# Kernel optimization log

Measured on AMD Instinct MI355X. Metric: run time of the kernel, lower is better.

## Reference

```python
import jax, jax.numpy as jnp
import numpy as np

IN_DIM = 1024
HID = 256
OUT_DIM = 1000
NUM_BINS = 51
BATCH = 2048
N_LEGAL = 200


def setup_inputs() -> dict:
    key = jax.random.key(0)
    ks = jax.random.split(key, 12)
    s = lambda fan_in: 1.0 / np.sqrt(fan_in)
    u = lambda k, shp, b: jax.random.uniform(k, shp, jnp.float32, -b, b)
    return {
        "x": jax.random.normal(ks[0], (BATCH, IN_DIM), jnp.float32),
        # weights stored as [in, out] (math-equivalent to torch Linear)
        "w_in": u(ks[1], (IN_DIM, HID), s(IN_DIM)),
        "b_in": u(ks[2], (HID,), s(IN_DIM)),
        "w_ah": u(ks[3], (HID, HID), s(HID)),
        "b_ah": u(ks[4], (HID,), s(HID)),
        "w_ao": u(ks[5], (HID, OUT_DIM * NUM_BINS), s(HID)),
        "b_ao": u(ks[6], (OUT_DIM * NUM_BINS,), s(HID)),
        "w_vh": u(ks[7], (HID, HID), s(HID)),
        "b_vh": u(ks[8], (HID,), s(HID)),
        "w_vo": u(ks[9], (HID, NUM_BINS), s(HID)),
        "b_vo": u(ks[10], (NUM_BINS,), s(HID)),
        "v_range": jnp.linspace(-10.0, 10.0, NUM_BINS, dtype=jnp.float32),
        "possible_moves": jax.random.randint(ks[11], (BATCH, N_LEGAL), 0, OUT_DIM),
    }


def reference(x, w_in, b_in, w_ah, b_ah, w_ao, b_ao, w_vh, b_vh, w_vo, b_vo,
              v_range, possible_moves):
    B = x.shape[0]
    h = jax.nn.relu(x @ w_in + b_in)                       # [B, 256]
    adv_h = jax.nn.relu(h @ w_ah + b_ah)                   # [B, 256]
    val_h = jax.nn.relu(h @ w_vh + b_vh)                   # [B, 256]
    adv = (adv_h @ w_ao + b_ao).reshape(B, OUT_DIM, NUM_BINS)
    val = (val_h @ w_vo + b_vo).reshape(B, 1, NUM_BINS)
    q = val + adv - adv.mean(axis=1, keepdims=True)        # [B, A, bins]
    p = jnp.maximum(jax.nn.softmax(q, axis=2), 1e-5)       # softmax + clamp(min=1e-5)
    q_vals = jnp.sum(p * v_range, axis=2)                  # [B, A]
    # LegalSoftmax: per-row scatter of 1.0 at legal indices, vectorized
    mask = jnp.zeros((B, OUT_DIM), x.dtype).at[
        jnp.arange(B)[:, None], possible_moves].set(1.0)
    filtered = q_vals * mask
    # faithful to torch: any exact-zero entry (masked OR coincidental) -> -inf
    return jnp.where(filtered == 0, -jnp.inf, filtered)
```

## Files before the change

### kernel.cpp

```cpp
#include <hip/hip_runtime.h>
#include <cstdint>
#include <cstddef>

#define NB      2048
#define INDIM   1024
#define HID     256
#define NA      1000
#define BINS    51
#define NLEG    200
#define NPAIR   (NB*NLEG)
#define NBLK    256
#define PPB     (NPAIR/NBLK)

#define NEG_SENTINEL (-1.0e30f)

typedef float    f32x4  __attribute__((ext_vector_type(4)));
typedef __bf16   bf16x8 __attribute__((ext_vector_type(8)));
typedef unsigned short us8 __attribute__((ext_vector_type(8)));
typedef unsigned short us4 __attribute__((ext_vector_type(4)));
typedef unsigned long long u64x2 __attribute__((ext_vector_type(2)));

__device__ __forceinline__ unsigned short f2bf(float f) {
  union { float f; unsigned u; } v; v.f = f;
  return (unsigned short)((v.u + 0x7FFFu + ((v.u >> 16) & 1u)) >> 16);
}
__device__ __forceinline__ bf16x8 as_bf(us8 v) { return __builtin_bit_cast(bf16x8, v); }
__device__ __forceinline__ int imin(int a, int b) { return a < b ? a : b; }

__device__ __forceinline__ unsigned f2fp8x4(float a, float b, float c, float d) {
  int v = 0;
  v = __builtin_amdgcn_cvt_pk_fp8_f32(a, b, v, false);
  v = __builtin_amdgcn_cvt_pk_fp8_f32(c, d, v, true);
  return (unsigned)v;
}
__device__ __forceinline__ unsigned char f2fp8(float f) {
  int v = __builtin_amdgcn_cvt_pk_fp8_f32(f, 0.f, 0, false);
  return (unsigned char)(v & 0xff);
}
__device__ __forceinline__ float fp82f(unsigned char u) {
  return __builtin_amdgcn_cvt_f32_fp8((int)u, 0);
}

__global__ __launch_bounds__(256) void k_pre(
    const float* __restrict__ w_ao, unsigned char* __restrict__ wp8,
    float* __restrict__ wmean_acc,
    const float* __restrict__ w_in, const float* __restrict__ w_ah,
    const float* __restrict__ w_vh,
    unsigned short* __restrict__ w_inT, unsigned short* __restrict__ w_ahT,
    unsigned short* __restrict__ w_vhT,
    float* __restrict__ out, const int* __restrict__ pm,
    int* __restrict__ cnt,
    const float* __restrict__ x, unsigned short* __restrict__ x_bf) {
  __shared__ __align__(16) unsigned char smem[16320];
  int b = blockIdx.x, tid = threadIdx.x;
  if (b < 1000) {
    unsigned char* st = smem;
    int s = b & 7, a0 = (b >> 3) * 8;
    const float* wbase = w_ao + (size_t)(s * 32) * (NA * BINS) + a0 * BINS;
    for (int i = tid; i < 816; i += 256) {
      int kq = i / 102, c4 = i - kq * 102;
      const float* rp = wbase + (size_t)(kq * 4) * (NA * BINS) + c4 * 4;
      float4 f0 = *(const float4*)(rp);
      float4 f1 = *(const float4*)(rp + NA * BINS);
      float4 f2 = *(const float4*)(rp + 2 * NA * BINS);
      float4 f3 = *(const float4*)(rp + 3 * NA * BINS);
      unsigned pk0 = f2fp8x4(f0.x * 16.f, f0.y * 16.f, f0.z * 16.f, f0.w * 16.f);
      unsigned pk1 = f2fp8x4(f1.x * 16.f, f1.y * 16.f, f1.z * 16.f, f1.w * 16.f);
      unsigned pk2 = f2fp8x4(f2.x * 16.f, f2.y * 16.f, f2.z * 16.f, f2.w * 16.f);
      unsigned pk3 = f2fp8x4(f3.x * 16.f, f3.y * 16.f, f3.z * 16.f, f3.w * 16.f);
      unsigned s01lo = __builtin_amdgcn_perm(pk1, pk0, 0x05010400u);
      unsigned s01hi = __builtin_amdgcn_perm(pk1, pk0, 0x07030602u);
      unsigned s23lo = __builtin_amdgcn_perm(pk3, pk2, 0x05010400u);
      unsigned s23hi = __builtin_amdgcn_perm(pk3, pk2, 0x07030602u);
      unsigned o0 = __builtin_amdgcn_perm(s23lo, s01lo, 0x05040100u);
      unsigned o1 = __builtin_amdgcn_perm(s23lo, s01lo, 0x07060302u);
      unsigned o2 = __builtin_amdgcn_perm(s23hi, s01hi, 0x05040100u);
      unsigned o3 = __builtin_amdgcn_perm(s23hi, s01hi, 0x07060302u);
      int k4 = kq * 4;
      int swz = ((c4 >> 2) & 3) << 3;
      int kb = ((k4 & 24) ^ swz) + (k4 & 7);
      int cbase = c4 * 160;
      *(unsigned*)(st + cbase + kb)       = o0;
      *(unsigned*)(st + cbase + 40 + kb)  = o1;
      *(unsigned*)(st + cbase + 80 + kb)  = o2;
      *(unsigned*)(st + cbase + 120 + kb) = o3;
    }
    __syncthreads();
    for (int i = tid; i < 32 * 51; i += 256) {
      int r = i / 51, j = i - r * 51;
      float s8 = 0.f;
#pragma unroll
      for (int aL = 0; aL < 8; aL++) {
        int c = aL * 51 + j;
        s8 += fp82f(st[c * 40 + ((r & 24) ^ (((c >> 4) & 3) << 3)) + (r & 7)]);
      }
      atomicAdd(&wmean_acc[(size_t)(s * 32 + r) * BINS + j], s8);
    }
    int t4 = (tid >> 6) & 3, l = tid & 63;
    int col = t4 * 16 + (l & 15), kg = l >> 4;
    for (int aL = 0; aL < 8; aL++) {
      unsigned lo = 0, hi = 0;
      if (col < BINS) {
        int ci = aL * 51 + col;
        unsigned long long v8 = *(const unsigned long long*)(
            st + ci * 40 + ((kg * 8) ^ (((ci >> 4) & 3) << 3)));
        lo = (unsigned)v8; hi = (unsigned)(v8 >> 32);
      }
      uint2 v; v.x = lo; v.y = hi;
      *(uint2*)(wp8 + (size_t)(a0 + aL) * 16384 +
                (size_t)((s * 2 + (t4 >> 1)) * 64 + l) * 16 + (t4 & 1) * 8) = v;
    }
  } else if (b < 1384) {
    int bb = b - 1000;
    float (*tile)[33] = (float(*)[33])smem;
    const float* w; unsigned short* wT; int K, N, kt, nt;
    if (bb < 256)      { w = w_in; wT = w_inT; K = INDIM; N = HID; kt = bb & 31;        nt = bb >> 5; }
    else if (bb < 320) { w = w_ah; wT = w_ahT; K = HID;   N = HID; kt = (bb - 256) & 7; nt = (bb - 256) >> 3; }
    else               { w = w_vh; wT = w_vhT; K = HID;   N = HID; kt = (bb - 320) & 7; nt = (bb - 320) >> 3; }
    int k0 = kt * 32, n0 = nt * 32;
    int cr = tid >> 5, cc = tid & 31;
#pragma unroll
    for (int it = 0; it < 4; it++)
      tile[cr + it * 8][cc] = w[(size_t)(k0 + cr + it * 8) * N + n0 + cc];
    __syncthreads();
#pragma unroll
    for (int it = 0; it < 4; it++)
      wT[(size_t)(n0 + cr + it * 8) * K + k0 + cc] = f2bf(tile[cc][cr + it * 8]);
  } else if (b < 1884) {
    int base = (b - 1384) * 1024 + tid;
    float4 v = {NEG_SENTINEL, NEG_SENTINEL, NEG_SENTINEL, NEG_SENTINEL};
#pragma unroll
    for (int it = 0; it < 4; it++) ((float4*)out)[base + it * 256] = v;
  } else if (b < 2396) {
    int base4 = (b - 1884) * 1024 + tid;
#pragma unroll
    for (int it = 0; it < 4; it++) {
      float4 v = ((const float4*)x)[base4 + it * 256];
      us4 o;
      o[0] = f2bf(v.x); o[1] = f2bf(v.y); o[2] = f2bf(v.z); o[3] = f2bf(v.w);
      ((us4*)x_bf)[base4 + it * 256] = o;
    }
  } else {
    int* lh = (int*)smem;
    int blk = b - 2396;
    for (int i = tid; i < NA; i += 256) lh[i] = 0;
    __syncthreads();
    int base = blk * PPB;
    for (int i = tid; i < PPB; i += 256) atomicAdd(&lh[pm[base + i]], 1);
    __syncthreads();
    for (int a = tid; a < NA; a += 256) {
      int v = lh[a];
      if (v) atomicAdd(&cnt[a], v);
    }
  }
}

__global__ __launch_bounds__(256) void k_mid(
    const unsigned short* __restrict__ x_bf, const unsigned short* __restrict__ w_inT,
    const float* __restrict__ b_in, unsigned short* __restrict__ h_bf,
    const float* __restrict__ w_vo, const float* __restrict__ wmean_acc,
    const float* __restrict__ b_vo, const float* __restrict__ b_ao,
    unsigned short* __restrict__ Wc, float* __restrict__ bias_c,
    const int* __restrict__ cnt, int* __restrict__ off, int* __restrict__ cursor) {
  __shared__ __align__(16) char smem[1024];
  int b = blockIdx.x, tid = threadIdx.x;
  if (b < 512) {
    int w = tid >> 6, l = tid & 63, la = l & 15, g = l >> 4;
    int idx = b * 4 + w;
    int m0 = (idx & 127) * 16, n0 = (idx >> 7) * 16;
    f32x4 acc = {0.f, 0.f, 0.f, 0.f};
    const us8* Bp = (const us8*)(w_inT + (size_t)(n0 + la) * INDIM) + g;
    const us8* Ap = (const us8*)(x_bf + (size_t)(m0 + la) * INDIM) + g;
#pragma unroll 8
    for (int s = 0; s < 32; s++)
      acc = __builtin_amdgcn_mfma_f32_16x16x32_bf16(as_bf(Ap[s * 4]), as_bf(Bp[s * 4]),
                                                    acc, 0, 0, 0);
    float bb = b_in[n0 + la];
#pragma unroll
    for (int r = 0; r < 4; r++) {
      float v = fmaxf(acc[r] + bb, 0.f);
      h_bf[(size_t)(m0 + g * 4 + r) * HID + n0 + la] = f2bf(v);
    }
  } else if (b < 576) {
    float* sred = (float*)smem;
    int n = b - 512, t = tid;
    for (int k = t; k < 512; k += 256) {
      float v = 0.f;
      if (n < BINS)
        v = (k < 256) ? w_vo[(size_t)k * BINS + n]
                      : (-(0.001f / 16.f) * wmean_acc[(size_t)(k - 256) * BINS + n]);
      Wc[(size_t)n * 512 + k] = f2bf(v);
    }
    float acc = 0.f;
    if (n < BINS)
      for (int a = t; a < NA; a += 256) acc += b_ao[(size_t)a * BINS + n];
    sred[t] = acc;
    __syncthreads();
    for (int d = 128; d > 0; d >>= 1) { if (t < d) sred[t] += sred[t + d]; __syncthreads(); }
    if (t == 0) bias_c[n] = (n < BINS) ? (b_vo[n] - 0.001f * sred[0]) : 0.f;
  } else {
    int* s = (int*)smem;
    int t = tid, i0 = 4 * t;
    int v0 = (i0     < NA) ? cnt[i0]     : 0;
    int v1 = (i0 + 1 < NA) ? cnt[i0 + 1] : 0;
    int v2 = (i0 + 2 < NA) ? cnt[i0 + 2] : 0;
    int v3 = (i0 + 3 < NA) ? cnt[i0 + 3] : 0;
    int sum = v0 + v1 + v2 + v3;
    s[t] = sum;
    __syncthreads();
    for (int d = 1; d < 256; d <<= 1) {
      int u = (t >= d) ? s[t - d] : 0;
      __syncthreads();
      s[t] += u;
      __syncthreads();
    }
    int excl = s[t] - sum;
    if (i0     < NA) { off[i0]     = excl;                cursor[i0]     = excl; }
    if (i0 + 1 < NA) { off[i0 + 1] = excl + v0;           cursor[i0 + 1] = excl + v0; }
    if (i0 + 2 < NA) { off[i0 + 2] = excl + v0 + v1;      cursor[i0 + 2] = excl + v0 + v1; }
    if (i0 + 3 < NA) { off[i0 + 3] = excl + v0 + v1 + v2; cursor[i0 + 3] = excl + v0 + v1 + v2; }
  }
}

__global__ __launch_bounds__(256) void k_heads(
    const unsigned short* __restrict__ h,
    const unsigned short* __restrict__ wA, const float* __restrict__ bA,
    const unsigned short* __restrict__ wV, const float* __restrict__ bV,
    const unsigned short* __restrict__ Wc, const float* __restrict__ bias_c,
    unsigned char* __restrict__ Aext8, float* __restrict__ cbuf_f,
    const int* __restrict__ pm, int* __restrict__ cursor, int* __restrict__ rows) {
  __shared__ __align__(16) char smem[16896];
  int b = blockIdx.x, tid = threadIdx.x;
  if (b < 128) {
    unsigned short* aL = (unsigned short*)smem;
    unsigned short* vL = (unsigned short*)smem + 16 * 264;
    int w = tid >> 6, l = tid & 63, la = l & 15, g = l >> 4;
    int m0 = b * 16;
    const us8* Ap = (const us8*)(h + (size_t)(m0 + la) * HID) + g;
    us8 aF[8];
#pragma unroll
    for (int s = 0; s < 8; s++) aF[s] = Ap[s * 4];
#pragma unroll
    for (int part = 0; part < 2; part++) {
      const unsigned short* BT = part ? wV : wA;
      const float* bias = part ? bV : bA;
      unsigned short* oL = part ? vL : aL;
#pragma unroll
      for (int nt = 0; nt < 4; nt++) {
        int n0 = w * 64 + nt * 16;
        f32x4 acc = {0.f, 0.f, 0.f, 0.f};
        const us8* Bp = (const us8*)(BT + (size_t)(n0 + la) * HID) + g;
#pragma unroll
        for (int s = 0; s < 8; s++)
          acc = __builtin_amdgcn_mfma_f32_16x16x32_bf16(as_bf(aF[s]), as_bf(Bp[s * 4]),
                                                        acc, 0, 0, 0);
        float bb = bias[n0 + la];
#pragma unroll
        for (int r = 0; r < 4; r++) {
          float v = fmaxf(acc[r] + bb, 0.f);
          oL[(g * 4 + r) * 264 + n0 + la] = f2bf(v);
          if (part == 0)
            Aext8[(size_t)(m0 + g * 4 + r) * HID + n0 + la] = f2fp8(v);
        }
      }
    }
    __syncthreads();
    int n0c = w * 16;
    f32x4 acc = {0.f, 0.f, 0.f, 0.f};
    const us8* Vp  = (const us8*)(vL + la * 264) + g;
    const us8* Ap2 = (const us8*)(aL + la * 264) + g;
    const us8* BpV = (const us8*)(Wc + (size_t)(n0c + la) * 512) + g;
    const us8* BpA = (const us8*)(Wc + (size_t)(n0c + la) * 512 + 256) + g;
#pragma unroll
    for (int s = 0; s < 8; s++)
      acc = __builtin_amdgcn_mfma_f32_16x16x32_bf16(as_bf(Vp[s * 4]), as_bf(BpV[s * 4]),
                                                    acc, 0, 0, 0);
#pragma unroll
    for (int s = 0; s < 8; s++)
      acc = __builtin_amdgcn_mfma_f32_16x16x32_bf16(as_bf(Ap2[s * 4]), as_bf(BpA[s * 4]),
                                                    acc, 0, 0, 0);
    float bb = bias_c[n0c + la];
#pragma unroll
    for (int r = 0; r < 4; r++)
      cbuf_f[(size_t)(m0 + g * 4 + r) * 64 + n0c + la] = acc[r] + bb;
  } else {
    int* lc = (int*)smem;
    int* lbase = (int*)(smem + 4096);
    int blk = b - 128, t = tid;
    for (int i = t; i < NA; i += 256) lc[i] = 0;
    __syncthreads();
    int pbase = blk * PPB;
    for (int i = t; i < PPB; i += 256) atomicAdd(&lc[pm[pbase + i]], 1);
    __syncthreads();
    for (int i = t; i < NA; i += 256) {
      int v = lc[i];
      lbase[i] = v ? atomicAdd(&cursor[i], v) : 0;
      lc[i] = 0;
    }
    __syncthreads();
    for (int i = t; i < PPB; i += 256) {
      int a = pm[pbase + i];
      int r = atomicAdd(&lc[a], 1);
      rows[lbase[a] + r] = (pbase + i) / NLEG;
    }
  }
}

#define TILE_BODY(TILE, RA_) do {                                              \
  int rA = (RA_);                                                              \
  const long long* Ap = (const long long*)(Aext8 + (size_t)rA * HID) + g;      \
  const float4* cf = (const float4*)(cbuf_f + (size_t)rA * 64);                \
  long long a8[8];                                                             \
  _Pragma("unroll") for (int s = 0; s < 8; s++) a8[s] = Ap[s * 4];             \
  float4 cq0 = cf[g], cq1 = cf[4 + g], cq2 = cf[8 + g], cq3 = cf[12 + g];      \
  f32x4 acc0 = {0.f,0.f,0.f,0.f}, acc1 = {0.f,0.f,0.f,0.f};                    \
  f32x4 acc2 = {0.f,0.f,0.f,0.f}, acc3 = {0.f,0.f,0.f,0.f};                    \
  __builtin_amdgcn_s_setprio(1);                                               \
  _Pragma("unroll") for (int s = 0; s < 8; s++) {                              \
    u64x2 b01 = sBv[(s * 2) * 64 + l];                                         \
    u64x2 b23 = sBv[(s * 2 + 1) * 64 + l];                                     \
    acc0 = __builtin_amdgcn_mfma_f32_16x16x32_fp8_fp8(                         \
        (long long)b01[0], a8[s], acc0, 0, 0, 0);                              \
    acc1 = __builtin_amdgcn_mfma_f32_16x16x32_fp8_fp8(                         \
        (long long)b01[1], a8[s], acc1, 0, 0, 0);                              \
    acc2 = __builtin_amdgcn_mfma_f32_16x16x32_fp8_fp8(                         \
        (long long)b23[0], a8[s], acc2, 0, 0, 0);                              \
    acc3 = __builtin_amdgcn_mfma_f32_16x16x32_fp8_fp8(                         \
        (long long)b23[1], a8[s], acc3, 0, 0, 0);                              \
  }                                                                            \
  __builtin_amdgcn_s_setprio(0);                                               \
  float S = 0.f;                                                               \
  f32x4 e0, e1, e2, e3;                                                        \
  _Pragma("unroll") for (int r = 0; r < 4; r++) {                              \
    e0[r] = __expf(fmaf(acc0[r], 0.0625f, cq0[r] + bao0[r])); S += e0[r];      \
    e1[r] = __expf(fmaf(acc1[r], 0.0625f, cq1[r] + bao1[r])); S += e1[r];      \
    e2[r] = __expf(fmaf(acc2[r], 0.0625f, cq2[r] + bao2[r])); S += e2[r];      \
    e3[r] = __expf(fmaf(acc3[r], 0.0625f, cq3[r] + bao3[r])); S += e3[r];      \
  }                                                                            \
  S += __shfl_xor(S, 16); S += __shfl_xor(S, 32);                              \
  float inv = 1.f / S, qv = 0.f;                                               \
  _Pragma("unroll") for (int r = 0; r < 4; r++) {                              \
    int bin = g * 4 + r;                                                       \
    qv = fmaf(fmaxf(e0[r] * inv, 1e-5f), (float)bin * 0.4f - 10.f, qv);        \
    qv = fmaf(fmaxf(e1[r] * inv, 1e-5f), (float)(bin + 16) * 0.4f - 10.f, qv); \
    qv = fmaf(fmaxf(e2[r] * inv, 1e-5f), (float)(bin + 32) * 0.4f - 10.f, qv); \
    if (bin + 48 < BINS)                                                       \
      qv = fmaf(fmaxf(e3[r] * inv, 1e-5f), (float)(bin + 48) * 0.4f - 10.f, qv); \
  }                                                                            \
  qv += __shfl_xor(qv, 16); qv += __shfl_xor(qv, 32);                          \
  int gi = (TILE) * 16 + la;                                                   \
  if (g == 0 && gi < count)                                                    \
    out[(size_t)rA * NA + a] = (qv == 0.f) ? NEG_SENTINEL : qv;                \
} while (0)

__global__ __launch_bounds__(256) void k_main_mfma(
    const unsigned char* __restrict__ Aext8,
    const float* __restrict__ cbuf_f,
    const unsigned char* __restrict__ wp8,
    const float* __restrict__ b_ao,
    const int* __restrict__ cnt, const int* __restrict__ off,
    const int* __restrict__ rows,
    float* __restrict__ out) {
  __shared__ __align__(16) long long sB8[2048];
  const u64x2* sBv = (const u64x2*)sB8;
  int bx = blockIdx.x;
  int a = (bx & 7) * 125 + (bx >> 3);
  int count = cnt[a];
  int ntiles = (count + 15) >> 4;
  if ((int)(blockIdx.y * 4) >= ntiles) return;
  int tid = threadIdx.x;
  int w = tid >> 6, l = tid & 63, la = l & 15, g = l >> 4;
  int base = off[a];
  int t0 = blockIdx.y * 4 + w;

  int rQ0 = rows[base + imin( t0       * 16 + la, count - 1)];
  int rQ1 = rows[base + imin((t0 + 16) * 16 + la, count - 1)];

  const float* baop = b_ao + (size_t)a * BINS;
  f32x4 bao0, bao1, bao2, bao3;
#pragma unroll
  for (int r = 0; r < 4; r++) {
    int bin = g * 4 + r;
    bao0[r] = baop[bin];
    bao1[r] = baop[bin + 16];
    bao2[r] = baop[bin + 32];
    bao3[r] = (bin + 48 < BINS) ? baop[bin + 48] : NEG_SENTINEL;
  }

  const u64x2* wpa = (const u64x2*)(wp8 + (size_t)a * 16384);
#pragma unroll
  for (int i = 0; i < 4; i++) ((u64x2*)sB8)[tid + i * 256] = wpa[tid + i * 256];
  __syncthreads();

  if (t0      < ntiles) TILE_BODY(t0,      rQ0);
  if (t0 + 16 < ntiles) TILE_BODY(t0 + 16, rQ1);
  for (int tile = t0 + 32; tile < ntiles; tile += 16) {
    int rAt = rows[base + imin(tile * 16 + la, count - 1)];
    TILE_BODY(tile, rAt);
  }
}

extern "C" void kernel_launch(void* const* d_in, const int* in_sizes, int n_in,
                              void* d_out, int out_size, void* d_ws, size_t ws_size,
                              hipStream_t stream) {
  (void)in_sizes; (void)n_in; (void)out_size; (void)ws_size;
  const float* x     = (const float*)d_in[0];
  const float* w_in  = (const float*)d_in[1];
  const float* b_in  = (const float*)d_in[2];
  const float* w_ah  = (const float*)d_in[3];
  const float* b_ah  = (const float*)d_in[4];
  const float* w_ao  = (const float*)d_in[5];
  const float* b_ao  = (const float*)d_in[6];
  const float* w_vh  = (const float*)d_in[7];
  const float* b_vh  = (const float*)d_in[8];
  const float* w_vo  = (const float*)d_in[9];
  const float* b_vo  = (const float*)d_in[10];
  const int*   pm    = (const int*)d_in[12];
  float* out = (float*)d_out;

  char* p = (char*)d_ws;
  unsigned char*  wp8     = (unsigned char*)p;  p += (size_t)NA * 32 * 512;
  unsigned char*  Aext8   = (unsigned char*)p;  p += (size_t)NB * HID;
  unsigned short* h_bf    = (unsigned short*)p; p += (size_t)NB * HID * 2;
  unsigned short* w_inT   = (unsigned short*)p; p += (size_t)HID * INDIM * 2;
  unsigned short* w_ahT   = (unsigned short*)p; p += (size_t)HID * HID * 2;
  unsigned short* w_vhT   = (unsigned short*)p; p += (size_t)HID * HID * 2;
  unsigned short* Wc      = (unsigned short*)p; p += (size_t)64 * 512 * 2;
  unsigned short* x_bf    = (unsigned short*)p; p += (size_t)NB * INDIM * 2;
  float* bias_c = (float*)p; p += 64 * 4;
  float* cbuf_f = (float*)p; p += (size_t)NB * 64 * 4;
  float* wmean  = (float*)p; p += 13056 * 4;
  int* cnt    = (int*)p; p += NA * 4;
  int* off    = (int*)p; p += NA * 4;
  int* cursor = (int*)p; p += (size_t)NA * 4 + 240;
  int* rows   = (int*)p; p += (size_t)NPAIR * 4 + 256;

  hipMemsetAsync(wmean, 0, (13056 + NA) * sizeof(float), stream);

  k_pre<<<2652, 256, 0, stream>>>(w_ao, wp8, wmean, w_in, w_ah, w_vh,
                                  w_inT, w_ahT, w_vhT, out, pm, cnt, x, x_bf);
  k_mid<<<577, 256, 0, stream>>>(x_bf, w_inT, b_in, h_bf,
                                 w_vo, wmean, b_vo, b_ao, Wc, bias_c,
                                 cnt, off, cursor);
  k_heads<<<384, 256, 0, stream>>>(h_bf, w_ahT, b_ah, w_vhT, b_vh,
                                   Wc, bias_c, Aext8, cbuf_f,
                                   pm, cursor, rows);
  k_main_mfma<<<dim3(1000, 4), 256, 0, stream>>>(Aext8, cbuf_f, wp8, b_ao,
                                                 cnt, off, rows, out);
}
```

Baseline: 209.6 us.

## Fuse four pipeline kernels into one persistent cooperative kernel with grid syncs

```diff
diff --git a/kernel.cpp b/kernel.cpp
--- a/kernel.cpp
+++ b/kernel.cpp
@@ -1,6 +1,9 @@
 #include <hip/hip_runtime.h>
+#include <hip/hip_cooperative_groups.h>
 #include <cstdint>
 #include <cstddef>
+
+namespace cg = cooperative_groups;
 
 #define NB      2048
 #define INDIM   1024
@@ -9,8 +12,7 @@
 #define BINS    51
 #define NLEG    200
 #define NPAIR   (NB*NLEG)
-#define NBLK    256
-#define PPB     (NPAIR/NBLK)
+#define PPB     (NPAIR/256)
 
 #define NEG_SENTINEL (-1.0e30f)
 
@@ -41,268 +43,275 @@
   return __builtin_amdgcn_cvt_f32_fp8((int)u, 0);
 }
 
-__global__ __launch_bounds__(256) void k_pre(
+
+__device__ __forceinline__ void body_pack(
+    int b, unsigned char* st, int tid,
     const float* __restrict__ w_ao, unsigned char* __restrict__ wp8,
-    float* __restrict__ wmean_acc,
+    float* __restrict__ wmean_acc) {
+  int s = b & 7, a0 = (b >> 3) * 8;
+  const float* wbase = w_ao + (size_t)(s * 32) * (NA * BINS) + a0 * BINS;
+  for (int i = tid; i < 816; i += 256) {
+    int kq = i / 102, c4 = i - kq * 102;
+    const float* rp = wbase + (size_t)(kq * 4) * (NA * BINS) + c4 * 4;
+    float4 f0 = *(const float4*)(rp);
+    float4 f1 = *(const float4*)(rp + NA * BINS);
+    float4 f2 = *(const float4*)(rp + 2 * NA * BINS);
+    float4 f3 = *(const float4*)(rp + 3 * NA * BINS);
+    unsigned pk0 = f2fp8x4(f0.x * 16.f, f0.y * 16.f, f0.z * 16.f, f0.w * 16.f);
+    unsigned pk1 = f2fp8x4(f1.x * 16.f, f1.y * 16.f, f1.z * 16.f, f1.w * 16.f);
+    unsigned pk2 = f2fp8x4(f2.x * 16.f, f2.y * 16.f, f2.z * 16.f, f2.w * 16.f);
+    unsigned pk3 = f2fp8x4(f3.x * 16.f, f3.y * 16.f, f3.z * 16.f, f3.w * 16.f);
+    unsigned s01lo = __builtin_amdgcn_perm(pk1, pk0, 0x05010400u);
+    unsigned s01hi = __builtin_amdgcn_perm(pk1, pk0, 0x07030602u);
+    unsigned s23lo = __builtin_amdgcn_perm(pk3, pk2, 0x05010400u);
+    unsigned s23hi = __builtin_amdgcn_perm(pk3, pk2, 0x07030602u);
+    unsigned o0 = __builtin_amdgcn_perm(s23lo, s01lo, 0x05040100u);
+    unsigned o1 = __builtin_amdgcn_perm(s23lo, s01lo, 0x07060302u);
+    unsigned o2 = __builtin_amdgcn_perm(s23hi, s01hi, 0x05040100u);
+    unsigned o3 = __builtin_amdgcn_perm(s23hi, s01hi, 0x07060302u);
+    int k4 = kq * 4;
+    int swz = ((c4 >> 2) & 3) << 3;
+    int kb = ((k4 & 24) ^ swz) + (k4 & 7);
+    int cbase = c4 * 160;
+    *(unsigned*)(st + cbase + kb)       = o0;
+    *(unsigned*)(st + cbase + 40 + kb)  = o1;
+    *(unsigned*)(st + cbase + 80 + kb)  = o2;
+    *(unsigned*)(st + cbase + 120 + kb) = o3;
+  }
+  __syncthreads();
+  for (int i = tid; i < 32 * 51; i += 256) {
+    int r = i / 51, j = i - r * 51;
+    float s8 = 0.f;
+#pragma unroll
+    for (int aL = 0; aL < 8; aL++) {
+      int c = aL * 51 + j;
+      s8 += fp82f(st[c * 40 + ((r & 24) ^ (((c >> 4) & 3) << 3)) + (r & 7)]);
+    }
+    atomicAdd(&wmean_acc[(size_t)(s * 32 + r) * BINS + j], s8);
+  }
+  int t4 = (tid >> 6) & 3, l = tid & 63;
+  int col = t4 * 16 + (l & 15), kg = l >> 4;
+  for (int aL = 0; aL < 8; aL++) {
+    unsigned lo = 0, hi = 0;
+    if (col < BINS) {
+      int ci = aL * 51 + col;
+      unsigned long long v8 = *(const unsigned long long*)(
+          st + ci * 40 + ((kg * 8) ^ (((ci >> 4) & 3) << 3)));
+      lo = (unsigned)v8; hi = (unsigned)(v8 >> 32);
+    }
+    uint2 v; v.x = lo; v.y = hi;
+    *(uint2*)(wp8 + (size_t)(a0 + aL) * 16384 +
+              (size_t)((s * 2 + (t4 >> 1)) * 64 + l) * 16 + (t4 & 1) * 8) = v;
+  }
+}
+
+__device__ __forceinline__ void body_transpose(
+    int bb, unsigned char* smem, int tid,
     const float* __restrict__ w_in, const float* __restrict__ w_ah,
     const float* __restrict__ w_vh,
     unsigned short* __restrict__ w_inT, unsigned short* __restrict__ w_ahT,
-    unsigned short* __restrict__ w_vhT,
-    float* __restrict__ out, const int* __restrict__ pm,
-    int* __restrict__ cnt,
-    const float* __restrict__ x, unsigned short* __restrict__ x_bf) {
-  __shared__ __align__(16) unsigned char smem[16320];
-  int b = blockIdx.x, tid = threadIdx.x;
-  if (b < 1000) {
-    unsigned char* st = smem;
-    int s = b & 7, a0 = (b >> 3) * 8;
-    const float* wbase = w_ao + (size_t)(s * 32) * (NA * BINS) + a0 * BINS;
-    for (int i = tid; i < 816; i += 256) {
-      int kq = i / 102, c4 = i - kq * 102;
-      const float* rp = wbase + (size_t)(kq * 4) * (NA * BINS) + c4 * 4;
-      float4 f0 = *(const float4*)(rp);
-      float4 f1 = *(const float4*)(rp + NA * BINS);
-      float4 f2 = *(const float4*)(rp + 2 * NA * BINS);
-      float4 f3 = *(const float4*)(rp + 3 * NA * BINS);
-      unsigned pk0 = f2fp8x4(f0.x * 16.f, f0.y * 16.f, f0.z * 16.f, f0.w * 16.f);
-      unsigned pk1 = f2fp8x4(f1.x * 16.f, f1.y * 16.f, f1.z * 16.f, f1.w * 16.f);
-      unsigned pk2 = f2fp8x4(f2.x * 16.f, f2.y * 16.f, f2.z * 16.f, f2.w * 16.f);
-      unsigned pk3 = f2fp8x4(f3.x * 16.f, f3.y * 16.f, f3.z * 16.f, f3.w * 16.f);
-      unsigned s01lo = __builtin_amdgcn_perm(pk1, pk0, 0x05010400u);
-      unsigned s01hi = __builtin_amdgcn_perm(pk1, pk0, 0x07030602u);
-      unsigned s23lo = __builtin_amdgcn_perm(pk3, pk2, 0x05010400u);
-      unsigned s23hi = __builtin_amdgcn_perm(pk3, pk2, 0x07030602u);
-      unsigned o0 = __builtin_amdgcn_perm(s23lo, s01lo, 0x05040100u);
-      unsigned o1 = __builtin_amdgcn_perm(s23lo, s01lo, 0x07060302u);
-      unsigned o2 = __builtin_amdgcn_perm(s23hi, s01hi, 0x05040100u);
-      unsigned o3 = __builtin_amdgcn_perm(s23hi, s01hi, 0x07060302u);
-      int k4 = kq * 4;
-      int swz = ((c4 >> 2) & 3) << 3;
-      int kb = ((k4 & 24) ^ swz) + (k4 & 7);
-      int cbase = c4 * 160;
-      *(unsigned*)(st + cbase + kb)       = o0;
-      *(unsigned*)(st + cbase + 40 + kb)  = o1;
-      *(unsigned*)(st + cbase + 80 + kb)  = o2;
-      *(unsigned*)(st + cbase + 120 + kb) = o3;
-    }
-    __syncthreads();
-    for (int i = tid; i < 32 * 51; i += 256) {
-      int r = i / 51, j = i - r * 51;
-      float s8 = 0.f;
-#pragma unroll
-      for (int aL = 0; aL < 8; aL++) {
-        int c = aL * 51 + j;
-        s8 += fp82f(st[c * 40 + ((r & 24) ^ (((c >> 4) & 3) << 3)) + (r & 7)]);
-      }
-      atomicAdd(&wmean_acc[(size_t)(s * 32 + r) * BINS + j], s8);
-    }
-    int t4 = (tid >> 6) & 3, l = tid & 63;
-    int col = t4 * 16 + (l & 15), kg = l >> 4;
-    for (int aL = 0; aL < 8; aL++) {
-      unsigned lo = 0, hi = 0;
-      if (col < BINS) {
-        int ci = aL * 51 + col;
-        unsigned long long v8 = *(const unsigned long long*)(
-            st + ci * 40 + ((kg * 8) ^ (((ci >> 4) & 3) << 3)));
-        lo = (unsigned)v8; hi = (unsigned)(v8 >> 32);
-      }
-      uint2 v; v.x = lo; v.y = hi;
-      *(uint2*)(wp8 + (size_t)(a0 + aL) * 16384 +
-                (size_t)((s * 2 + (t4 >> 1)) * 64 + l) * 16 + (t4 & 1) * 8) = v;
-    }
-  } else if (b < 1384) {
-    int bb = b - 1000;
-    float (*tile)[33] = (float(*)[33])smem;
-    const float* w; unsigned short* wT; int K, N, kt, nt;
-    if (bb < 256)      { w = w_in; wT = w_inT; K = INDIM; N = HID; kt = bb & 31;        nt = bb >> 5; }
-    else if (bb < 320) { w = w_ah; wT = w_ahT; K = HID;   N = HID; kt = (bb - 256) & 7; nt = (bb - 256) >> 3; }
-    else               { w = w_vh; wT = w_vhT; K = HID;   N = HID; kt = (bb - 320) & 7; nt = (bb - 320) >> 3; }
-    int k0 = kt * 32, n0 = nt * 32;
-    int cr = tid >> 5, cc = tid & 31;
-#pragma unroll
-    for (int it = 0; it < 4; it++)
-      tile[cr + it * 8][cc] = w[(size_t)(k0 + cr + it * 8) * N + n0 + cc];
-    __syncthreads();
-#pragma unroll
-    for (int it = 0; it < 4; it++)
-      wT[(size_t)(n0 + cr + it * 8) * K + k0 + cc] = f2bf(tile[cc][cr + it * 8]);
-  } else if (b < 1884) {
-    int base = (b - 1384) * 1024 + tid;
-    float4 v = {NEG_SENTINEL, NEG_SENTINEL, NEG_SENTINEL, NEG_SENTINEL};
-#pragma unroll
-    for (int it = 0; it < 4; it++) ((float4*)out)[base + it * 256] = v;
-  } else if (b < 2396) {
-    int base4 = (b - 1884) * 1024 + tid;
-#pragma unroll
-    for (int it = 0; it < 4; it++) {
-      float4 v = ((const float4*)x)[base4 + it * 256];
-      us4 o;
-      o[0] = f2bf(v.x); o[1] = f2bf(v.y); o[2] = f2bf(v.z); o[3] = f2bf(v.w);
-      ((us4*)x_bf)[base4 + it * 256] = o;
-    }
-  } else {
-    int* lh = (int*)smem;
-    int blk = b - 2396;
-    for (int i = tid; i < NA; i += 256) lh[i] = 0;
-    __syncthreads();
-    int base = blk * PPB;
-    for (int i = tid; i < PPB; i += 256) atomicAdd(&lh[pm[base + i]], 1);
-    __syncthreads();
-    for (int a = tid; a < NA; a += 256) {
-      int v = lh[a];
-      if (v) atomicAdd(&cnt[a], v);
-    }
-  }
-}
-
-__global__ __launch_bounds__(256) void k_mid(
+    unsigned short* __restrict__ w_vhT) {
+  float (*tile)[33] = (float(*)[33])smem;
+  const float* w; unsigned short* wT; int K, N, kt, nt;
+  if (bb < 256)      { w = w_in; wT = w_inT; K = INDIM; N = HID; kt = bb & 31;        nt = bb >> 5; }
+  else if (bb < 320) { w = w_ah; wT = w_ahT; K = HID;   N = HID; kt = (bb - 256) & 7; nt = (bb - 256) >> 3; }
+  else               { w = w_vh; wT = w_vhT; K = HID;   N = HID; kt = (bb - 320) & 7; nt = (bb - 320) >> 3; }
+  int k0 = kt * 32, n0 = nt * 32;
+  int cr = tid >> 5, cc = tid & 31;
+#pragma unroll
+  for (int it = 0; it < 4; it++)
+    tile[cr + it * 8][cc] = w[(size_t)(k0 + cr + it * 8) * N + n0 + cc];
+  __syncthreads();
+#pragma unroll
+  for (int it = 0; it < 4; it++)
+    wT[(size_t)(n0 + cr + it * 8) * K + k0 + cc] = f2bf(tile[cc][cr + it * 8]);
+}
+
+__device__ __forceinline__ void body_outinit(int bb, int tid, float* __restrict__ out) {
+  int base = bb * 1024 + tid;
+  float4 v = {NEG_SENTINEL, NEG_SENTINEL, NEG_SENTINEL, NEG_SENTINEL};
+#pragma unroll
+  for (int it = 0; it < 4; it++) ((float4*)out)[base + it * 256] = v;
+}
+
+__device__ __forceinline__ void body_xbf(
+    int bb, int tid, const float* __restrict__ x, unsigned short* __restrict__ x_bf) {
+  int base4 = bb * 1024 + tid;
+#pragma unroll
+  for (int it = 0; it < 4; it++) {
+    float4 v = ((const float4*)x)[base4 + it * 256];
+    us4 o;
+    o[0] = f2bf(v.x); o[1] = f2bf(v.y); o[2] = f2bf(v.z); o[3] = f2bf(v.w);
+    ((us4*)x_bf)[base4 + it * 256] = o;
+  }
+}
+
+__device__ __forceinline__ void body_count(
+    int blk, unsigned char* smem, int tid,
+    const int* __restrict__ pm, int* __restrict__ cnt) {
+  int* lh = (int*)smem;
+  for (int i = tid; i < NA; i += 256) lh[i] = 0;
+  __syncthreads();
+  int base = blk * PPB;
+  for (int i = tid; i < PPB; i += 256) atomicAdd(&lh[pm[base + i]], 1);
+  __syncthreads();
+  for (int a = tid; a < NA; a += 256) {
+    int v = lh[a];
+    if (v) atomicAdd(&cnt[a], v);
+  }
+}
+
+__device__ __forceinline__ void body_hgemm(
+    int b, int tid,
     const unsigned short* __restrict__ x_bf, const unsigned short* __restrict__ w_inT,
-    const float* __restrict__ b_in, unsigned short* __restrict__ h_bf,
+    const float* __restrict__ b_in, unsigned short* __restrict__ h_bf) {
+  int w = tid >> 6, l = tid & 63, la = l & 15, g = l >> 4;
+  int idx = b * 4 + w;
+  int m0 = (idx & 127) * 16, n0 = (idx >> 7) * 16;
+  f32x4 acc = {0.f, 0.f, 0.f, 0.f};
+  const us8* Bp = (const us8*)(w_inT + (size_t)(n0 + la) * INDIM) + g;
+  const us8* Ap = (const us8*)(x_bf + (size_t)(m0 + la) * INDIM) + g;
+#pragma unroll 8
+  for (int s = 0; s < 32; s++)
+    acc = __builtin_amdgcn_mfma_f32_16x16x32_bf16(as_bf(Ap[s * 4]), as_bf(Bp[s * 4]),
+                                                  acc, 0, 0, 0);
+  float bb = b_in[n0 + la];
+#pragma unroll
+  for (int r = 0; r < 4; r++) {
+    float v = fmaxf(acc[r] + bb, 0.f);
+    h_bf[(size_t)(m0 + g * 4 + r) * HID + n0 + la] = f2bf(v);
+  }
+}
+
+__device__ __forceinline__ void body_wcprep(
+    int n, unsigned char* smem, int tid,
     const float* __restrict__ w_vo, const float* __restrict__ wmean_acc,
     const float* __restrict__ b_vo, const float* __restrict__ b_ao,
-    unsigned short* __restrict__ Wc, float* __restrict__ bias_c,
+    unsigned short* __restrict__ Wc, float* __restrict__ bias_c) {
+  float* sred = (float*)smem;
+  int t = tid;
+  for (int k = t; k < 512; k += 256) {
+    float v = 0.f;
+    if (n < BINS)
+      v = (k < 256) ? w_vo[(size_t)k * BINS + n]
+                    : (-(0.001f / 16.f) * wmean_acc[(size_t)(k - 256) * BINS + n]);
+    Wc[(size_t)n * 512 + k] = f2bf(v);
+  }
+  float acc = 0.f;
+  if (n < BINS)
+    for (int a = t; a < NA; a += 256) acc += b_ao[(size_t)a * BINS + n];
+  sred[t] = acc;
+  __syncthreads();
+  for (int d = 128; d > 0; d >>= 1) { if (t < d) sred[t] += sred[t + d]; __syncthreads(); }
+  if (t == 0) bias_c[n] = (n < BINS) ? (b_vo[n] - 0.001f * sred[0]) : 0.f;
+}
+
+__device__ __forceinline__ void body_offscan(
+    unsigned char* smem, int tid,
     const int* __restrict__ cnt, int* __restrict__ off, int* __restrict__ cursor) {
-  __shared__ __align__(16) char smem[1024];
-  int b = blockIdx.x, tid = threadIdx.x;
-  if (b < 512) {
-    int w = tid >> 6, l = tid & 63, la = l & 15, g = l >> 4;
-    int idx = b * 4 + w;
-    int m0 = (idx & 127) * 16, n0 = (idx >> 7) * 16;
-    f32x4 acc = {0.f, 0.f, 0.f, 0.f};
-    const us8* Bp = (const us8*)(w_inT + (size_t)(n0 + la) * INDIM) + g;
-    const us8* Ap = (const us8*)(x_bf + (size_t)(m0 + la) * INDIM) + g;
-#pragma unroll 8
-    for (int s = 0; s < 32; s++)
-      acc = __builtin_amdgcn_mfma_f32_16x16x32_bf16(as_bf(Ap[s * 4]), as_bf(Bp[s * 4]),
-                                                    acc, 0, 0, 0);
-    float bb = b_in[n0 + la];
-#pragma unroll
-    for (int r = 0; r < 4; r++) {
-      float v = fmaxf(acc[r] + bb, 0.f);
-      h_bf[(size_t)(m0 + g * 4 + r) * HID + n0 + la] = f2bf(v);
-    }
-  } else if (b < 576) {
-    float* sred = (float*)smem;
-    int n = b - 512, t = tid;
-    for (int k = t; k < 512; k += 256) {
-      float v = 0.f;
-      if (n < BINS)
-        v = (k < 256) ? w_vo[(size_t)k * BINS + n]
-                      : (-(0.001f / 16.f) * wmean_acc[(size_t)(k - 256) * BINS + n]);
-      Wc[(size_t)n * 512 + k] = f2bf(v);
-    }
-    float acc = 0.f;
-    if (n < BINS)
-      for (int a = t; a < NA; a += 256) acc += b_ao[(size_t)a * BINS + n];
-    sred[t] = acc;
+  int* s = (int*)smem;
+  int t = tid, i0 = 4 * t;
+  int v0 = (i0     < NA) ? cnt[i0]     : 0;
+  int v1 = (i0 + 1 < NA) ? cnt[i0 + 1] : 0;
+  int v2 = (i0 + 2 < NA) ? cnt[i0 + 2] : 0;
+  int v3 = (i0 + 3 < NA) ? cnt[i0 + 3] : 0;
+  int sum = v0 + v1 + v2 + v3;
+  s[t] = sum;
+  __syncthreads();
+  for (int d = 1; d < 256; d <<= 1) {
+    int u = (t >= d) ? s[t - d] : 0;
     __syncthreads();
-    for (int d = 128; d > 0; d >>= 1) { if (t < d) sred[t] += sred[t + d]; __syncthreads(); }
-    if (t == 0) bias_c[n] = (n < BINS) ? (b_vo[n] - 0.001f * sred[0]) : 0.f;
-  } else {
-    int* s = (int*)smem;
-    int t = tid, i0 = 4 * t;
-    int v0 = (i0     < NA) ? cnt[i0]     : 0;
-    int v1 = (i0 + 1 < NA) ? cnt[i0 + 1] : 0;
-    int v2 = (i0 + 2 < NA) ? cnt[i0 + 2] : 0;
-    int v3 = (i0 + 3 < NA) ? cnt[i0 + 3] : 0;
-    int sum = v0 + v1 + v2 + v3;
-    s[t] = sum;
+    s[t] += u;
     __syncthreads();
-    for (int d = 1; d < 256; d <<= 1) {
-      int u = (t >= d) ? s[t - d] : 0;
-      __syncthreads();
-      s[t] += u;
-      __syncthreads();
-    }
-    int excl = s[t] - sum;
-    if (i0     < NA) { off[i0]     = excl;                cursor[i0]     = excl; }
-    if (i0 + 1 < NA) { off[i0 + 1] = excl + v0;           cursor[i0 + 1] = excl + v0; }
-    if (i0 + 2 < NA) { off[i0 + 2] = excl + v0 + v1;      cursor[i0 + 2] = excl + v0 + v1; }
-    if (i0 + 3 < NA) { off[i0 + 3] = excl + v0 + v1 + v2; cursor[i0 + 3] = excl + v0 + v1 + v2; }
-  }
-}
-
-__global__ __launch_bounds__(256) void k_heads(
+  }
+  int excl = s[t] - sum;
+  if (i0     < NA) { off[i0]     = excl;                cursor[i0]     = excl; }
+  if (i0 + 1 < NA) { off[i0 + 1] = excl + v0;           cursor[i0 + 1] = excl + v0; }
+  if (i0 + 2 < NA) { off[i0 + 2] = excl + v0 + v1;      cursor[i0 + 2] = excl + v0 + v1; }
+  if (i0 + 3 < NA) { off[i0 + 3] = excl + v0 + v1 + v2; cursor[i0 + 3] = excl + v0 + v1 + v2; }
+}
+
+__device__ __forceinline__ void body_heads(
+    int b, unsigned char* smem, int tid,
     const unsigned short* __restrict__ h,
     const unsigned short* __restrict__ wA, const float* __restrict__ bA,
     const unsigned short* __restrict__ wV, const float* __restrict__ bV,
     const unsigned short* __restrict__ Wc, const float* __restrict__ bias_c,
-    unsigned char* __restrict__ Aext8, float* __restrict__ cbuf_f,
-    const int* __restrict__ pm, int* __restrict__ cursor, int* __restrict__ rows) {
-  __shared__ __align__(16) char smem[16896];
-  int b = blockIdx.x, tid = threadIdx.x;
-  if (b < 128) {
-    unsigned short* aL = (unsigned short*)smem;
-    unsigned short* vL = (unsigned short*)smem + 16 * 264;
-    int w = tid >> 6, l = tid & 63, la = l & 15, g = l >> 4;
-    int m0 = b * 16;
-    const us8* Ap = (const us8*)(h + (size_t)(m0 + la) * HID) + g;
-    us8 aF[8];
-#pragma unroll
-    for (int s = 0; s < 8; s++) aF[s] = Ap[s * 4];
-#pragma unroll
-    for (int part = 0; part < 2; part++) {
-      const unsigned short* BT = part ? wV : wA;
-      const float* bias = part ? bV : bA;
-      unsigned short* oL = part ? vL : aL;
-#pragma unroll
-      for (int nt = 0; nt < 4; nt++) {
-        int n0 = w * 64 + nt * 16;
-        f32x4 acc = {0.f, 0.f, 0.f, 0.f};
-        const us8* Bp = (const us8*)(BT + (size_t)(n0 + la) * HID) + g;
-#pragma unroll
-        for (int s = 0; s < 8; s++)
-          acc = __builtin_amdgcn_mfma_f32_16x16x32_bf16(as_bf(aF[s]), as_bf(Bp[s * 4]),
-                                                        acc, 0, 0, 0);
-        float bb = bias[n0 + la];
-#pragma unroll
-        for (int r = 0; r < 4; r++) {
-          float v = fmaxf(acc[r] + bb, 0.f);
-          oL[(g * 4 + r) * 264 + n0 + la] = f2bf(v);
-          if (part == 0)
-            Aext8[(size_t)(m0 + g * 4 + r) * HID + n0 + la] = f2fp8(v);
-        }
+    unsigned char* __restrict__ Aext8, float* __restrict__ cbuf_f) {
+  unsigned short* aL = (unsigned short*)smem;
+  unsigned short* vL = (unsigned short*)smem + 16 * 264;
+  int w = tid >> 6, l = tid & 63, la = l & 15, g = l >> 4;
+  int m0 = b * 16;
+  const us8* Ap = (const us8*)(h + (size_t)(m0 + la) * HID) + g;
+  us8 aF[8];
+#pragma unroll
+  for (int s = 0; s < 8; s++) aF[s] = Ap[s * 4];
+#pragma unroll
+  for (int part = 0; part < 2; part++) {
+    const unsigned short* BT = part ? wV : wA;
+    const float* bias = part ? bV : bA;
+    unsigned short* oL = part ? vL : aL;
+#pragma unroll
+    for (int nt = 0; nt < 4; nt++) {
+      int n0 = w * 64 + nt * 16;
+      f32x4 acc = {0.f, 0.f, 0.f, 0.f};
+      const us8* Bp = (const us8*)(BT + (size_t)(n0 + la) * HID) + g;
+#pragma unroll
+      for (int s = 0; s < 8; s++)
+        acc = __builtin_amdgcn_mfma_f32_16x16x32_bf16(as_bf(aF[s]), as_bf(Bp[s * 4]),
+                                                      acc, 0, 0, 0);
+      float bb = bias[n0 + la];
+#pragma unroll
+      for (int r = 0; r < 4; r++) {
+        float v = fmaxf(acc[r] + bb, 0.f);
+        oL[(g * 4 + r) * 264 + n0 + la] = f2bf(v);
+        if (part == 0)
+          Aext8[(size_t)(m0 + g * 4 + r) * HID + n0 + la] = f2fp8(v);
       }
     }
-    __syncthreads();
-    int n0c = w * 16;
-    f32x4 acc = {0.f, 0.f, 0.f, 0.f};
-    const us8* Vp  = (const us8*)(vL + la * 264) + g;
-    const us8* Ap2 = (const us8*)(aL + la * 264) + g;
-    const us8* BpV = (const us8*)(Wc + (size_t)(n0c + la) * 512) + g;
-    const us8* BpA = (const us8*)(Wc + (size_t)(n0c + la) * 512 + 256) + g;
-#pragma unroll
-    for (int s = 0; s < 8; s++)
-      acc = __builtin_amdgcn_mfma_f32_16x16x32_bf16(as_bf(Vp[s * 4]), as_bf(BpV[s * 4]),
-                                                    acc, 0, 0, 0);
-#pragma unroll
-    for (int s = 0; s < 8; s++)
-      acc = __builtin_amdgcn_mfma_f32_16x16x32_bf16(as_bf(Ap2[s * 4]), as_bf(BpA[s * 4]),
-                                                    acc, 0, 0, 0);
-    float bb = bias_c[n0c + la];
-#pragma unroll
-    for (int r = 0; r < 4; r++)
-      cbuf_f[(size_t)(m0 + g * 4 + r) * 64 + n0c + la] = acc[r] + bb;
-  } else {
-    int* lc = (int*)smem;
-    int* lbase = (int*)(smem + 4096);
-    int blk = b - 128, t = tid;
-    for (int i = t; i < NA; i += 256) lc[i] = 0;
-    __syncthreads();
-    int pbase = blk * PPB;
-    for (int i = t; i < PPB; i += 256) atomicAdd(&lc[pm[pbase + i]], 1);
-    __syncthreads();
-    for (int i = t; i < NA; i += 256) {
-      int v = lc[i];
-      lbase[i] = v ? atomicAdd(&cursor[i], v) : 0;
-      lc[i] = 0;
-    }
-    __syncthreads();
-    for (int i = t; i < PPB; i += 256) {
-      int a = pm[pbase + i];
-      int r = atomicAdd(&lc[a], 1);
-      rows[lbase[a] + r] = (pbase + i) / NLEG;
-    }
+  }
+  __syncthreads();
+  int n0c = w * 16;
+  f32x4 acc = {0.f, 0.f, 0.f, 0.f};
+  const us8* Vp  = (const us8*)(vL + la * 264) + g;
+  const us8* Ap2 = (const us8*)(aL + la * 264) + g;
+  const us8* BpV = (const us8*)(Wc + (size_t)(n0c + la) * 512) + g;
+  const us8* BpA = (const us8*)(Wc + (size_t)(n0c + la) * 512 + 256) + g;
+#pragma unroll
+  for (int s = 0; s < 8; s++)
+    acc = __builtin_amdgcn_mfma_f32_16x16x32_bf16(as_bf(Vp[s * 4]), as_bf(BpV[s * 4]),
+                                                  acc, 0, 0, 0);
+#pragma unroll
+  for (int s = 0; s < 8; s++)
+    acc = __builtin_amdgcn_mfma_f32_16x16x32_bf16(as_bf(Ap2[s * 4]), as_bf(BpA[s * 4]),
+                                                  acc, 0, 0, 0);
+  float bb = bias_c[n0c + la];
+#pragma unroll
+  for (int r = 0; r < 4; r++)
+    cbuf_f[(size_t)(m0 + g * 4 + r) * 64 + n0c + la] = acc[r] + bb;
+}
+
+__device__ __forceinline__ void body_scatter(
+    int blk, unsigned char* smem, int tid,
+    const int* __restrict__ pm, int* __restrict__ cursor, int* __restrict__ rows) {
+  int* lc = (int*)smem;
+  int* lbase = (int*)(smem + 4096);
+  int t = tid;
+  for (int i = t; i < NA; i += 256) lc[i] = 0;
+  __syncthreads();
+  int pbase = blk * PPB;
+  for (int i = t; i < PPB; i += 256) atomicAdd(&lc[pm[pbase + i]], 1);
+  __syncthreads();
+  for (int i = t; i < NA; i += 256) {
+    int v = lc[i];
+    lbase[i] = v ? atomicAdd(&cursor[i], v) : 0;
+    lc[i] = 0;
+  }
+  __syncthreads();
+  for (int i = t; i < PPB; i += 256) {
+    int a = pm[pbase + i];
+    int r = atomicAdd(&lc[a], 1);
+    rows[lbase[a] + r] = (pbase + i) / NLEG;
   }
 }
 
@@ -353,28 +362,26 @@
     out[(size_t)rA * NA + a] = (qv == 0.f) ? NEG_SENTINEL : qv;                \
 } while (0)
 
-__global__ __launch_bounds__(256) void k_main_mfma(
-    const unsigned char* __restrict__ Aext8,
-    const float* __restrict__ cbuf_f,
-    const unsigned char* __restrict__ wp8,
-    const float* __restrict__ b_ao,
+__device__ __forceinline__ void body_main(
+    int bx, int y, unsigned char* smem, int tid,
+    const unsigned char* __restrict__ Aext8, const float* __restrict__ cbuf_f,
+    const unsigned char* __restrict__ wp8, const float* __restrict__ b_ao,
     const int* __restrict__ cnt, const int* __restrict__ off,
-    const int* __restrict__ rows,
-    float* __restrict__ out) {
-  __shared__ __align__(16) long long sB8[2048];
-  const u64x2* sBv = (const u64x2*)sB8;
-  int bx = blockIdx.x;
+    const int* __restrict__ rows, float* __restrict__ out) {
+  long long* sB8 = (long long*)smem;
+  const u64x2* sBv = (const u64x2*)smem;
   int a = (bx & 7) * 125 + (bx >> 3);
   int count = cnt[a];
   int ntiles = (count + 15) >> 4;
-  if ((int)(blockIdx.y * 4) >= ntiles) return;
-  int tid = threadIdx.x;
+  if (count == 0 || y * 4 >= ntiles) return;
   int w = tid >> 6, l = tid & 63, la = l & 15, g = l >> 4;
   int base = off[a];
-  int t0 = blockIdx.y * 4 + w;
+  int t0 = y * 4 + w;
 
   int rQ0 = rows[base + imin( t0       * 16 + la, count - 1)];
-  int rQ1 = rows[base + imin((t0 + 16) * 16 + la, count - 1)];
+  int rQ1 = rows[base + imin((t0 +  8) * 16 + la, count - 1)];
+  int rQ2 = rows[base + imin((t0 + 16) * 16 + la, count - 1)];
+  int rQ3 = rows[base + imin((t0 + 24) * 16 + la, count - 1)];
 
   const float* baop = b_ao + (size_t)a * BINS;
   f32x4 bao0, bao1, bao2, bao3;
@@ -393,11 +400,114 @@
   __syncthreads();
 
   if (t0      < ntiles) TILE_BODY(t0,      rQ0);
-  if (t0 + 16 < ntiles) TILE_BODY(t0 + 16, rQ1);
-  for (int tile = t0 + 32; tile < ntiles; tile += 16) {
+  if (t0 +  8 < ntiles) TILE_BODY(t0 +  8, rQ1);
+  if (t0 + 16 < ntiles) TILE_BODY(t0 + 16, rQ2);
+  if (t0 + 24 < ntiles) TILE_BODY(t0 + 24, rQ3);
+  for (int tile = t0 + 32; tile < ntiles; tile += 8) {
     int rAt = rows[base + imin(tile * 16 + la, count - 1)];
     TILE_BODY(tile, rAt);
   }
+}
+
+__global__ __launch_bounds__(256, 5) void k_fused(
+    const float* w_ao, const float* w_in, const float* b_in,
+    const float* w_ah, const float* b_ah, const float* w_vh, const float* b_vh,
+    const float* w_vo, const float* b_vo, const float* b_ao,
+    const float* x, const int* pm, float* out,
+    unsigned char* wp8, unsigned char* Aext8, unsigned short* h_bf,
+    unsigned short* w_inT, unsigned short* w_ahT, unsigned short* w_vhT,
+    unsigned short* Wc, unsigned short* x_bf, float* bias_c, float* cbuf_f,
+    float* wmean, int* cnt, int* off, int* cursor, int* rows) {
+  __shared__ __align__(16) unsigned char smem[16896];
+  int tid = threadIdx.x;
+  int nblk = gridDim.x;
+
+  for (int vb = blockIdx.x; vb < 2652; vb += nblk) {
+    __syncthreads();
+    if (vb < 1000)      body_pack(vb, smem, tid, w_ao, wp8, wmean);
+    else if (vb < 1384) body_transpose(vb - 1000, smem, tid, w_in, w_ah, w_vh,
+                                       w_inT, w_ahT, w_vhT);
+    else if (vb < 1884) body_outinit(vb - 1384, tid, out);
+    else if (vb < 2396) body_xbf(vb - 1884, tid, x, x_bf);
+    else                body_count(vb - 2396, smem, tid, pm, cnt);
+  }
+  cg::this_grid().sync();
+
+  for (int vb = blockIdx.x; vb < 577; vb += nblk) {
+    __syncthreads();
+    if (vb < 512)      body_hgemm(vb, tid, x_bf, w_inT, b_in, h_bf);
+    else if (vb < 576) body_wcprep(vb - 512, smem, tid, w_vo, wmean, b_vo, b_ao,
+                                   Wc, bias_c);
+    else               body_offscan(smem, tid, cnt, off, cursor);
+  }
+  cg::this_grid().sync();
+
+  for (int vb = blockIdx.x; vb < 384; vb += nblk) {
+    __syncthreads();
+    if (vb < 128) body_heads(vb, smem, tid, h_bf, w_ahT, b_ah, w_vhT, b_vh,
+                             Wc, bias_c, Aext8, cbuf_f);
+    else          body_scatter(vb - 128, smem, tid, pm, cursor, rows);
+  }
+  cg::this_grid().sync();
+
+  for (int vb = blockIdx.x; vb < 2000; vb += nblk) {
+    __syncthreads();
+    int y = vb >= 1000;
+    body_main(y ? vb - 1000 : vb, y, smem, tid, Aext8, cbuf_f, wp8, b_ao,
+              cnt, off, rows, out);
+  }
+}
+
+__global__ __launch_bounds__(256) void k_pre(
+    const float* w_ao, unsigned char* wp8, float* wmean,
+    const float* w_in, const float* w_ah, const float* w_vh,
+    unsigned short* w_inT, unsigned short* w_ahT, unsigned short* w_vhT,
+    float* out, const int* pm, int* cnt,
+    const float* x, unsigned short* x_bf) {
+  __shared__ __align__(16) unsigned char smem[16896];
+  int b = blockIdx.x, tid = threadIdx.x;
+  if (b < 1000)      body_pack(b, smem, tid, w_ao, wp8, wmean);
+  else if (b < 1384) body_transpose(b - 1000, smem, tid, w_in, w_ah, w_vh,
+                                    w_inT, w_ahT, w_vhT);
+  else if (b < 1884) body_outinit(b - 1384, tid, out);
+  else if (b < 2396) body_xbf(b - 1884, tid, x, x_bf);
+  else               body_count(b - 2396, smem, tid, pm, cnt);
+}
+
+__global__ __launch_bounds__(256) void k_mid(
+    const unsigned short* x_bf, const unsigned short* w_inT,
+    const float* b_in, unsigned short* h_bf,
+    const float* w_vo, const float* wmean, const float* b_vo, const float* b_ao,
+    unsigned short* Wc, float* bias_c,
+    const int* cnt, int* off, int* cursor) {
+  __shared__ __align__(16) unsigned char smem[16896];
+  int b = blockIdx.x, tid = threadIdx.x;
+  if (b < 512)      body_hgemm(b, tid, x_bf, w_inT, b_in, h_bf);
+  else if (b < 576) body_wcprep(b - 512, smem, tid, w_vo, wmean, b_vo, b_ao,
+                                Wc, bias_c);
+  else              body_offscan(smem, tid, cnt, off, cursor);
+}
+
+__global__ __launch_bounds__(256) void k_heads(
+    const unsigned short* h_bf, const unsigned short* w_ahT, const float* b_ah,
+    const unsigned short* w_vhT, const float* b_vh,
+    const unsigned short* Wc, const float* bias_c,
+    unsigned char* Aext8, float* cbuf_f,
+    const int* pm, int* cursor, int* rows) {
+  __shared__ __align__(16) unsigned char smem[16896];
+  int b = blockIdx.x, tid = threadIdx.x;
+  if (b < 128) body_heads(b, smem, tid, h_bf, w_ahT, b_ah, w_vhT, b_vh,
+                          Wc, bias_c, Aext8, cbuf_f);
+  else         body_scatter(b - 128, smem, tid, pm, cursor, rows);
+}
+
+__global__ __launch_bounds__(256) void k_main_mfma(
+    const unsigned char* Aext8, const float* cbuf_f, const unsigned char* wp8,
+    const float* b_ao, const int* cnt, const int* off, const int* rows,
+    float* out) {
+  __shared__ __align__(16) unsigned char smem[16896];
+  body_main(blockIdx.x, blockIdx.y, smem, threadIdx.x, Aext8, cbuf_f, wp8,
+            b_ao, cnt, off, rows, out);
 }
 
 extern "C" void kernel_launch(void* const* d_in, const int* in_sizes, int n_in,
@@ -419,14 +529,14 @@
   float* out = (float*)d_out;
 
   char* p = (char*)d_ws;
-  unsigned char*  wp8     = (unsigned char*)p;  p += (size_t)NA * 32 * 512;
-  unsigned char*  Aext8   = (unsigned char*)p;  p += (size_t)NB * HID;
-  unsigned short* h_bf    = (unsigned short*)p; p += (size_t)NB * HID * 2;
-  unsigned short* w_inT   = (unsigned short*)p; p += (size_t)HID * INDIM * 2;
-  unsigned short* w_ahT   = (unsigned short*)p; p += (size_t)HID * HID * 2;
-  unsigned short* w_vhT   = (unsigned short*)p; p += (size_t)HID * HID * 2;
-  unsigned short* Wc      = (unsigned short*)p; p += (size_t)64 * 512 * 2;
-  unsigned short* x_bf    = (unsigned short*)p; p += (size_t)NB * INDIM * 2;
+  unsigned char*  wp8    = (unsigned char*)p;  p += (size_t)NA * 32 * 512;
+  unsigned char*  Aext8  = (unsigned char*)p;  p += (size_t)NB * HID;
+  unsigned short* h_bf   = (unsigned short*)p; p += (size_t)NB * HID * 2;
+  unsigned short* w_inT  = (unsigned short*)p; p += (size_t)HID * INDIM * 2;
+  unsigned short* w_ahT  = (unsigned short*)p; p += (size_t)HID * HID * 2;
+  unsigned short* w_vhT  = (unsigned short*)p; p += (size_t)HID * HID * 2;
+  unsigned short* Wc     = (unsigned short*)p; p += (size_t)64 * 512 * 2;
+  unsigned short* x_bf   = (unsigned short*)p; p += (size_t)NB * INDIM * 2;
   float* bias_c = (float*)p; p += 64 * 4;
   float* cbuf_f = (float*)p; p += (size_t)NB * 64 * 4;
   float* wmean  = (float*)p; p += 13056 * 4;
@@ -437,14 +547,51 @@
 
   hipMemsetAsync(wmean, 0, (13056 + NA) * sizeof(float), stream);
 
-  k_pre<<<2652, 256, 0, stream>>>(w_ao, wp8, wmean, w_in, w_ah, w_vh,
-                                  w_inT, w_ahT, w_vhT, out, pm, cnt, x, x_bf);
-  k_mid<<<577, 256, 0, stream>>>(x_bf, w_inT, b_in, h_bf,
-                                 w_vo, wmean, b_vo, b_ao, Wc, bias_c,
-                                 cnt, off, cursor);
-  k_heads<<<384, 256, 0, stream>>>(h_bf, w_ahT, b_ah, w_vhT, b_vh,
-                                   Wc, bias_c, Aext8, cbuf_f,
-                                   pm, cursor, rows);
-  k_main_mfma<<<dim3(1000, 4), 256, 0, stream>>>(Aext8, cbuf_f, wp8, b_ao,
-                                                 cnt, off, rows, out);
-}
+  static int s_grid = 0;
+  if (s_grid == 0) {
+    int nb = 0;
+    if (hipOccupancyMaxActiveBlocksPerMultiprocessor(&nb, k_fused, 256, 0)
+            != hipSuccess || nb <= 0) {
+      s_grid = -1;
+    } else {
+      int ncu = 256, dev = 0;
+      hipDeviceProp_t prop;
+      if (hipGetDevice(&dev) == hipSuccess &&
+          hipGetDeviceProperties(&prop, dev) == hipSuccess)
+        ncu = prop.multiProcessorCount;
+      int g = nb * ncu;
+      g = (g / 8) * 8;
+      if (g > 2648) g = 2648;
+      s_grid = (g >= 8) ? g : -1;
+    }
+  }
+
+  bool coop_done = false;
+  if (s_grid > 0) {
+    void* kargs[] = {
+      (void*)&w_ao, (void*)&w_in, (void*)&b_in, (void*)&w_ah, (void*)&b_ah,
+      (void*)&w_vh, (void*)&b_vh, (void*)&w_vo, (void*)&b_vo, (void*)&b_ao,
+      (void*)&x, (void*)&pm, (void*)&out,
+      (void*)&wp8, (void*)&Aext8, (void*)&h_bf,
+      (void*)&w_inT, (void*)&w_ahT, (void*)&w_vhT,
+      (void*)&Wc, (void*)&x_bf, (void*)&bias_c, (void*)&cbuf_f,
+      (void*)&wmean, (void*)&cnt, (void*)&off, (void*)&cursor, (void*)&rows};
+    hipError_t e = hipLaunchCooperativeKernel(
+        k_fused, dim3(s_grid), dim3(256), kargs, 0, stream);
+    if (e == hipSuccess) coop_done = true;
+    else s_grid = -1;
+  }
+
+  if (!coop_done) {
+    k_pre<<<2652, 256, 0, stream>>>(w_ao, wp8, wmean, w_in, w_ah, w_vh,
+                                    w_inT, w_ahT, w_vhT, out, pm, cnt, x, x_bf);
+    k_mid<<<577, 256, 0, stream>>>(x_bf, w_inT, b_in, h_bf,
+                                   w_vo, wmean, b_vo, b_ao, Wc, bias_c,
+                                   cnt, off, cursor);
+    k_heads<<<384, 256, 0, stream>>>(h_bf, w_ahT, b_ah, w_vhT, b_vh,
+                                     Wc, bias_c, Aext8, cbuf_f,
+                                     pm, cursor, rows);
+    k_main_mfma<<<dim3(1000, 2), 256, 0, stream>>>(Aext8, cbuf_f, wp8, b_ao,
+                                                   cnt, off, rows, out);
+  }
+}
```

After: 434.7 us. 2.07x slower.
